# Kernel optimization log

Hardware: AMD Instinct MI355X
Metric: run time of the kernel (lower is better)

Reference implementation:

```python
import jax, jax.numpy as jnp
import numpy as np

GROUP_SIZE = 128


def setup_inputs() -> dict:
    key = jax.random.key(0)
    k0, k1, k2, k3 = jax.random.split(key, 4)
    B, S, I, O, G = 4, 2048, 4096, 11008, GROUP_SIZE
    x = jax.random.normal(k0, (B, S, I), dtype=jnp.float32)
    # int4 values in [-8, 7]
    qweight = jax.random.randint(k1, (O, I), -8, 8, dtype=jnp.int32)
    # group-wise positive scales, shape [O, I // G]
    scales = jax.random.uniform(k2, (O, I // G), dtype=jnp.float32,
                                minval=1e-3, maxval=2e-2)
    bias = jax.random.normal(k3, (O,), dtype=jnp.float32) * 0.01
    return {"x": x, "qweight": qweight, "scales": scales, "bias": bias}


def reference(x, qweight, scales, bias):
    # bits == 4, quantized path: group-wise dequant then linear
    O, I = qweight.shape
    G = GROUP_SIZE
    w = qweight.reshape(O, I // G, G).astype(x.dtype) * scales[:, :, None].astype(x.dtype)
    w = w.reshape(O, I)  # dequantized weight [O, I]
    # F.linear: y = x @ w.T + bias
    return jnp.einsum('bsi,oi->bso', x, w) + bias.astype(x.dtype)
```

## Files before the change

### kernel.cpp

```cpp
#include <hip/hip_runtime.h>
#include <hip/hip_bf16.h>


typedef __bf16 bf16_t;
typedef __bf16 bf16x8 __attribute__((ext_vector_type(8)));
typedef float f32x4 __attribute__((ext_vector_type(4)));
typedef int ix4 __attribute__((ext_vector_type(4)));
typedef __attribute__((address_space(3))) unsigned char lds_byte;
typedef __attribute__((address_space(1))) unsigned char gmem_byte;

__global__ void prep_kernel(const float* __restrict__ x, int* __restrict__ xq,
                            float* __restrict__ sx,
                            const int* __restrict__ qw, const float* __restrict__ sc,
                            float* __restrict__ tw, int* __restrict__ wq,
                            int M, int I, int NG) {
  __shared__ float red[256];
  const int b = blockIdx.x;
  const int t = threadIdx.x;
  if (b < M) {
    const float* row = x + (size_t)b * I;
    float mx = 0.f;
    for (int c = t * 4; c < I; c += 1024) {
      const float4 f = *reinterpret_cast<const float4*>(row + c);
      mx = fmaxf(mx, fmaxf(fmaxf(fabsf(f.x), fabsf(f.y)), fmaxf(fabsf(f.z), fabsf(f.w))));
    }
    red[t] = mx;
    __syncthreads();
#pragma unroll
    for (int s = 128; s > 0; s >>= 1) {
      if (t < s) red[t] = fmaxf(red[t], red[t + s]);
      __syncthreads();
    }
    const float rm = fmaxf(red[0], 1e-30f);
    if (t == 0) sx[b] = rm * (1.f / 127.f);
    const float inv = 127.f / rm;
    int* orow = xq + (size_t)b * (I >> 2);
    for (int c = t * 4; c < I; c += 1024) {
      const float4 f = *reinterpret_cast<const float4*>(row + c);
      const int b0 = (int)rintf(f.x * inv), b1 = (int)rintf(f.y * inv);
      const int b2 = (int)rintf(f.z * inv), b3 = (int)rintf(f.w * inv);
      orow[c >> 2] = (b0 & 255) | ((b1 & 255) << 8) | ((b2 & 255) << 16) | (b3 << 24);
    }
  } else {
    const int n = b - M;
    const float* srow = sc + (size_t)n * NG;
    float mx = 0.f;
    for (int g = t; g < NG; g += 256) mx = fmaxf(mx, srow[g]);
    red[t] = mx;
    __syncthreads();
#pragma unroll
    for (int s = 128; s > 0; s >>= 1) {
      if (t < s) red[t] = fmaxf(red[t], red[t + s]);
      __syncthreads();
    }
    const float tn = fmaxf(red[0], 1e-30f) * (8.f / 127.f);
    if (t == 0) tw[n] = tn;
    const float itn = 1.f / tn;
    const int* qrow = qw + (size_t)n * I;
    int* orow = wq + (size_t)n * (I >> 2);
    for (int k0 = t * 16; k0 < I; k0 += 4096) {
      const float f = srow[k0 >> 7] * itn;
      const int4* p = reinterpret_cast<const int4*>(qrow + k0);
      const int4 q0 = p[0], q1 = p[1], q2 = p[2], q3 = p[3];
      int v[16];
      v[0] = (int)rintf((float)q0.x * f); v[1] = (int)rintf((float)q0.y * f);
      v[2] = (int)rintf((float)q0.z * f); v[3] = (int)rintf((float)q0.w * f);
      v[4] = (int)rintf((float)q1.x * f); v[5] = (int)rintf((float)q1.y * f);
      v[6] = (int)rintf((float)q1.z * f); v[7] = (int)rintf((float)q1.w * f);
      v[8] = (int)rintf((float)q2.x * f); v[9] = (int)rintf((float)q2.y * f);
      v[10] = (int)rintf((float)q2.z * f); v[11] = (int)rintf((float)q2.w * f);
      v[12] = (int)rintf((float)q3.x * f); v[13] = (int)rintf((float)q3.y * f);
      v[14] = (int)rintf((float)q3.z * f); v[15] = (int)rintf((float)q3.w * f);
      int4 o;
      o.x = (v[0] & 255) | ((v[1] & 255) << 8) | ((v[2] & 255) << 16) | (v[3] << 24);
      o.y = (v[4] & 255) | ((v[5] & 255) << 8) | ((v[6] & 255) << 16) | (v[7] << 24);
      o.z = (v[8] & 255) | ((v[9] & 255) << 8) | ((v[10] & 255) << 16) | (v[11] << 24);
      o.w = (v[12] & 255) | ((v[13] & 255) << 8) | ((v[14] & 255) << 16) | (v[15] << 24);
      *reinterpret_cast<int4*>(orow + (k0 >> 2)) = o;
    }
  }
}


#define WAITV(n) asm volatile("s_waitcnt vmcnt(" #n ")" ::: "memory")
#define WAITL(n) asm volatile("s_waitcnt lgkmcnt(" #n ")" ::: "memory")
#define BAR() __builtin_amdgcn_s_barrier()
#define SETP(n) __builtin_amdgcn_s_setprio(n)

#define RD_T(DB) do { \
  _Pragma("unroll") \
  for (int m_ = 0; m_ < 2; ++m_) { \
    aF[m_][0] = *reinterpret_cast<const ix4*>(&ldsb[(DB) + aRd + (unsigned)(m_ * 16) * 128u + ks0]); \
    aF[m_][1] = *reinterpret_cast<const ix4*>(&ldsb[(DB) + aRd + (unsigned)(m_ * 16) * 128u + ks1]); \
  } \
  _Pragma("unroll") \
  for (int n_ = 0; n_ < 4; ++n_) { \
    bF[n_][0] = *reinterpret_cast<const ix4*>(&ldsb[(DB) + 16384u + bRd + (unsigned)(n_ * 16) * 128u + ks0]); \
    bF[n_][1] = *reinterpret_cast<const ix4*>(&ldsb[(DB) + 16384u + bRd + (unsigned)(n_ * 16) * 128u + ks1]); \
  } \
} while (0)

#define STG(BASE, P, tau) do { \
  __builtin_amdgcn_global_load_lds((const gmem_byte*)((P) + (size_t)(tau) * 128), \
                                   (lds_byte*)&ldsb[(BASE) + wOff], 16, 0, 0); \
  __builtin_amdgcn_global_load_lds((const gmem_byte*)((P) + (size_t)64 * K + (size_t)(tau) * 128), \
                                   (lds_byte*)&ldsb[(BASE) + 8192u + wOff], 16, 0, 0); \
} while (0)

#define MM_T() do { \
  _Pragma("unroll") \
  for (int m_ = 0; m_ < 2; ++m_) \
  _Pragma("unroll") \
  for (int n_ = 0; n_ < 4; ++n_) { \
    acc[m_][n_] = __builtin_amdgcn_mfma_i32_16x16x64_i8(aF[m_][0], bF[n_][0], acc[m_][n_], 0, 0, 0); \
    acc[m_][n_] = __builtin_amdgcn_mfma_i32_16x16x64_i8(aF[m_][1], bF[n_][1], acc[m_][n_], 0, 0, 0); \
  } \
} while (0)

__launch_bounds__(512, 4)
__global__ void gemm128_i8_kernel(const char* __restrict__ A, const char* __restrict__ B,
                                  const float* __restrict__ sx, const float* __restrict__ tw,
                                  const float* __restrict__ bias, float* __restrict__ C,
                                  int M, int N, int K) {
  __shared__ __align__(16) unsigned char ldsb[65536];

  const int tid = threadIdx.x;
  const int lane = tid & 63;
  const int w = tid >> 6;
  const int wr = w >> 1;
  const int wc = w & 1;

  const int MT = M >> 7;
  int mt, nt;
  const int bid = blockIdx.x;
  if ((MT & 7) == 0) {
    const int xcd = bid & 7, idx = bid >> 3;
    const int mpx = MT >> 3;
    nt = idx / mpx;
    mt = xcd * mpx + (idx - nt * mpx);
  } else {
    mt = bid % MT;
    nt = bid / MT;
  }
  const int m0 = mt << 7, n0 = nt << 7;

  const int srow8 = lane >> 3;
  const int scol16 = (lane & 7) ^ (srow8 & 7);
  const char* aP = A + (size_t)(m0 + w * 8 + srow8) * K + scol16 * 16;
  const char* bP = B + (size_t)(n0 + w * 8 + srow8) * K + scol16 * 16;
  const unsigned wOff = (unsigned)w * 1024u;

  const unsigned fr = lane & 15;
  const unsigned hi16 = (unsigned)lane >> 4;
  const unsigned sw_ = (fr & 7u) << 4;
  const unsigned ks0 = (hi16 * 16u) ^ sw_;
  const unsigned ks1 = (64u + hi16 * 16u) ^ sw_;
  const unsigned aRd = ((unsigned)(wr * 32) + fr) * 128u;
  const unsigned bRd = ((unsigned)(wc * 64) + fr) * 128u;

  ix4 acc[2][4];
#pragma unroll
  for (int i = 0; i < 2; ++i)
#pragma unroll
    for (int j = 0; j < 4; ++j) acc[i][j] = (ix4){0, 0, 0, 0};

  ix4 aF[2][2], bF[4][2];

  const int NITER = K >> 7;

  STG(0u, aP, 0); STG(16384u, bP, 0);
  STG(32768u, aP, 1); STG(49152u, bP, 1);
  WAITV(4);
  BAR();

  for (int it = 0; it < (NITER >> 1) - 1; ++it) {
    const int t = 2 * it;
    RD_T(0u);
    WAITL(0);
    BAR();
    STG(0u, aP, t + 2); STG(16384u, bP, t + 2);
    SETP(1); MM_T(); SETP(0);
    WAITV(4);
    BAR();
    RD_T(32768u);
    WAITL(0);
    BAR();
    STG(32768u, aP, t + 3); STG(49152u, bP, t + 3);
    SETP(1); MM_T(); SETP(0);
    WAITV(4);
    BAR();
  }
  {
    RD_T(0u);
    WAITV(0);
    BAR();
    WAITL(0);
    SETP(1); MM_T(); SETP(0);
    RD_T(32768u);
    WAITL(0);
    SETP(1); MM_T(); SETP(0);
  }

  const int row0 = m0 + wr * 32 + ((lane >> 4) << 2);
  const int col0 = n0 + wc * 64 + (lane & 15);
  float sxc[2][4];
#pragma unroll
  for (int m_ = 0; m_ < 2; ++m_) {
    const int rbase = row0 + m_ * 16;
#pragma unroll
    for (int r = 0; r < 4; ++r) sxc[m_][r] = sx[rbase + r];
  }
#pragma unroll
  for (int n_ = 0; n_ < 4; ++n_) {
    const int n = col0 + n_ * 16;
    const float tn = tw[n];
    const float bv = bias[n];
#pragma unroll
    for (int m_ = 0; m_ < 2; ++m_) {
      const int rbase = row0 + m_ * 16;
#pragma unroll
      for (int r = 0; r < 4; ++r)
        C[(size_t)(rbase + r) * N + n] = sxc[m_][r] * tn * (float)acc[m_][n_][r] + bv;
    }
  }
}

__global__ void cvt_x_kernel(const float* __restrict__ x, bf16_t* __restrict__ xb, long n8) {
  const long stride = (long)gridDim.x * blockDim.x;
  for (long i = (long)blockIdx.x * blockDim.x + threadIdx.x; i < n8; i += stride) {
    const float4* p = reinterpret_cast<const float4*>(x + i * 8);
    const float4 f0 = p[0];
    const float4 f1 = p[1];
    bf16x8 o;
    o[0] = (bf16_t)f0.x; o[1] = (bf16_t)f0.y; o[2] = (bf16_t)f0.z; o[3] = (bf16_t)f0.w;
    o[4] = (bf16_t)f1.x; o[5] = (bf16_t)f1.y; o[6] = (bf16_t)f1.z; o[7] = (bf16_t)f1.w;
    *reinterpret_cast<bf16x8*>(xb + i * 8) = o;
  }
}

__global__ void deq_w_kernel(const int* __restrict__ qw, const float* __restrict__ sc,
                             bf16_t* __restrict__ wb, int I, int G) {
  const int n = blockIdx.y;
  const int kb = blockIdx.x * blockDim.x + threadIdx.x;
  const int k = kb * 8;
  if (k >= I) return;
  const float s = sc[(size_t)n * (I / G) + k / G];
  const int4* qp = reinterpret_cast<const int4*>(qw + (size_t)n * I + k);
  const int4 q0 = qp[0];
  const int4 q1 = qp[1];
  bf16x8 o;
  o[0] = (bf16_t)((float)q0.x * s);
  o[1] = (bf16_t)((float)q0.y * s);
  o[2] = (bf16_t)((float)q0.z * s);
  o[3] = (bf16_t)((float)q0.w * s);
  o[4] = (bf16_t)((float)q1.x * s);
  o[5] = (bf16_t)((float)q1.y * s);
  o[6] = (bf16_t)((float)q1.z * s);
  o[7] = (bf16_t)((float)q1.w * s);
  *reinterpret_cast<bf16x8*>(wb + (size_t)n * I + k) = o;
}

#define BM 128
#define BK 32
__launch_bounds__(256)
__global__ void gemm_bt_kernel(const bf16_t* __restrict__ A, const bf16_t* __restrict__ B,
                               const float* __restrict__ bias, float* __restrict__ C,
                               int M, int N, int K) {
  __shared__ __align__(16) bf16_t As[2][BM * BK];
  __shared__ __align__(16) bf16_t Bs[2][BM * BK];
  const int tid = threadIdx.x;
  const int lane = tid & 63;
  const int w = tid >> 6;
  const int wr = w >> 1;
  const int wc = w & 1;
  const int m0 = blockIdx.y * BM;
  const int n0 = blockIdx.x * BM;
  const int srow = lane >> 2;
  const int schunk = lane & 3;
  f32x4 acc[4][4];
  const f32x4 zero = {0.f, 0.f, 0.f, 0.f};
#pragma unroll
  for (int i = 0; i < 4; ++i)
#pragma unroll
    for (int j = 0; j < 4; ++j) acc[i][j] = zero;
  const int nt = K / BK;
  auto stage = [&](int t, int buf) {
    const int k0 = t * BK;
#pragma unroll
    for (int j = 0; j < 2; ++j) {
      const int row = w * 32 + j * 16;
      const bf16_t* ga = A + (size_t)(m0 + row + srow) * K + k0 + schunk * 8;
      __builtin_amdgcn_global_load_lds((const gmem_byte*)ga, (lds_byte*)&As[buf][row * BK], 16, 0, 0);
      const bf16_t* gb = B + (size_t)(n0 + row + srow) * K + k0 + schunk * 8;
      __builtin_amdgcn_global_load_lds((const gmem_byte*)gb, (lds_byte*)&Bs[buf][row * BK], 16, 0, 0);
    }
  };
  auto compute = [&](int buf) {
    bf16x8 af[4], bfr[4];
    const int fr2 = lane & 15;
    const int kc = (lane >> 4) * 8;
#pragma unroll
    for (int i = 0; i < 4; ++i) {
      af[i] = *reinterpret_cast<const bf16x8*>(&As[buf][(wr * 64 + i * 16 + fr2) * BK + kc]);
      bfr[i] = *reinterpret_cast<const bf16x8*>(&Bs[buf][(wc * 64 + i * 16 + fr2) * BK + kc]);
    }
#pragma unroll
    for (int i = 0; i < 4; ++i)
#pragma unroll
      for (int j = 0; j < 4; ++j)
        acc[i][j] = __builtin_amdgcn_mfma_f32_16x16x32_bf16(af[i], bfr[j], acc[i][j], 0, 0, 0);
  };
  stage(0, 0);
  __syncthreads();
  int cur = 0;
  for (int t = 0; t < nt - 1; ++t) {
    stage(t + 1, cur ^ 1);
    compute(cur);
    __syncthreads();
    cur ^= 1;
  }
  compute(cur);
#pragma unroll
  for (int j = 0; j < 4; ++j) {
    const int n = n0 + wc * 64 + j * 16 + (lane & 15);
    const float bv = bias[n];
#pragma unroll
    for (int i = 0; i < 4; ++i) {
      const int mbase = m0 + wr * 64 + i * 16 + (lane >> 4) * 4;
#pragma unroll
      for (int r = 0; r < 4; ++r)
        C[(size_t)(mbase + r) * N + n] = acc[i][j][r] + bv;
    }
  }
}

extern "C" void kernel_launch(void* const* d_in, const int* in_sizes, int n_in,
                              void* d_out, int out_size, void* d_ws, size_t ws_size,
                              hipStream_t stream) {
  const float* x = (const float*)d_in[0];
  const int* qw = (const int*)d_in[1];
  const float* sc = (const float*)d_in[2];
  const float* bias = (const float*)d_in[3];
  float* out = (float*)d_out;

  const long O = in_sizes[3];
  const long I = in_sizes[1] / O;
  const long M = in_sizes[0] / I;
  const long G = I / (in_sizes[2] / O);
  const long NG = I / G;

  const size_t i8need = (size_t)(M + O) * I + 4 * (size_t)(M + O);
  const long NITER = I >> 7;
  const bool i8ok = ((M & 127) == 0) && ((O & 127) == 0) && ((I & 127) == 0) &&
                    (G == 128) && (NITER >= 4) && ((NITER & 1) == 0) &&
                    (ws_size >= i8need);
  if (i8ok) {
    char* xq = (char*)d_ws;
    char* wq = xq + (size_t)M * I;
    float* sx = (float*)(wq + (size_t)O * I);
    float* tw = sx + M;
    prep_kernel<<<(unsigned)(M + O), 256, 0, stream>>>(x, (int*)xq, sx, qw, sc, tw,
                                                       (int*)wq, (int)M, (int)I, (int)NG);
    const int nwg = (int)((M >> 7) * (O >> 7));
    gemm128_i8_kernel<<<nwg, 512, 0, stream>>>(xq, wq, sx, tw, bias, out, (int)M, (int)O, (int)I);
  } else {
    bf16_t* xb = (bf16_t*)d_ws;
    bf16_t* wb = xb + (size_t)M * I;
    if (ws_size < (size_t)(M + O) * I * sizeof(bf16_t)) return;
    cvt_x_kernel<<<2048, 256, 0, stream>>>(x, xb, M * I / 8);
    dim3 dgrid((unsigned)((I / 8 + 255) / 256), (unsigned)O);
    deq_w_kernel<<<dgrid, 256, 0, stream>>>(qw, sc, wb, (int)I, (int)G);
    dim3 ggrid((unsigned)(O / BM), (unsigned)(M / BM));
    gemm_bt_kernel<<<ggrid, 256, 0, stream>>>(xb, wb, bias, out, (int)M, (int)O, (int)I);
  }
}
```

Measured before the change: 483.1 us.

## Double-buffer B fragments in registers and interleave LDS reads with MFMAs

Splits the B fragment registers into two sets (even and odd tiles). The LDS reads for the next tile's B fragments are issued inside the MFMA cluster of the current tile, and sched_group_barrier hints pair two MFMAs with one LDS read. The A fragment read is moved to just after each cluster, and the barrier and wait structure is reworked around this software pipeline. The aim is to hide LDS read latency behind matrix math; in exchange it needs about 32 more VGPRs under a 4-waves-per-SIMD bound, which risks spills, and it waits for all outstanding global loads (vmcnt 0) before each barrier.

Result: slower. 515.2 us (+6.6%).

```diff
diff --git a/kernel.cpp b/kernel.cpp
--- a/kernel.cpp
+++ b/kernel.cpp
@@ -86,17 +86,36 @@
 #define WAITL(n) asm volatile("s_waitcnt lgkmcnt(" #n ")" ::: "memory")
 #define BAR() __builtin_amdgcn_s_barrier()
 #define SETP(n) __builtin_amdgcn_s_setprio(n)
-
-#define RD_T(DB) do { \
+#define SGB __builtin_amdgcn_sched_group_barrier
+
+#define RD_A(DB) do { \
   _Pragma("unroll") \
   for (int m_ = 0; m_ < 2; ++m_) { \
     aF[m_][0] = *reinterpret_cast<const ix4*>(&ldsb[(DB) + aRd + (unsigned)(m_ * 16) * 128u + ks0]); \
     aF[m_][1] = *reinterpret_cast<const ix4*>(&ldsb[(DB) + aRd + (unsigned)(m_ * 16) * 128u + ks1]); \
   } \
+} while (0)
+
+#define CLUSTER(BC, BN, DBN) do { \
   _Pragma("unroll") \
-  for (int n_ = 0; n_ < 4; ++n_) { \
-    bF[n_][0] = *reinterpret_cast<const ix4*>(&ldsb[(DB) + 16384u + bRd + (unsigned)(n_ * 16) * 128u + ks0]); \
-    bF[n_][1] = *reinterpret_cast<const ix4*>(&ldsb[(DB) + 16384u + bRd + (unsigned)(n_ * 16) * 128u + ks1]); \
+  for (int p_ = 0; p_ < 8; ++p_) { \
+    const int m_ = p_ >> 2, n_ = p_ & 3; \
+    acc[m_][n_] = __builtin_amdgcn_mfma_i32_16x16x64_i8(aF[m_][0], BC[n_][0], acc[m_][n_], 0, 0, 0); \
+    acc[m_][n_] = __builtin_amdgcn_mfma_i32_16x16x64_i8(aF[m_][1], BC[n_][1], acc[m_][n_], 0, 0, 0); \
+    const int rn_ = p_ >> 1, rs_ = p_ & 1; \
+    BN[rn_][rs_] = *reinterpret_cast<const ix4*>( \
+      &ldsb[(DBN) + 16384u + bRd + (unsigned)(rn_ * 16) * 128u + (rs_ ? ks1 : ks0)]); \
+  } \
+  _Pragma("unroll") \
+  for (int p_ = 0; p_ < 8; ++p_) { SGB(0x8, 2, 0); SGB(0x100, 1, 0); } \
+} while (0)
+
+#define CLUSTER_LAST(BC) do { \
+  _Pragma("unroll") \
+  for (int p_ = 0; p_ < 8; ++p_) { \
+    const int m_ = p_ >> 2, n_ = p_ & 3; \
+    acc[m_][n_] = __builtin_amdgcn_mfma_i32_16x16x64_i8(aF[m_][0], BC[n_][0], acc[m_][n_], 0, 0, 0); \
+    acc[m_][n_] = __builtin_amdgcn_mfma_i32_16x16x64_i8(aF[m_][1], BC[n_][1], acc[m_][n_], 0, 0, 0); \
   } \
 } while (0)
 
@@ -105,16 +124,6 @@
                                    (lds_byte*)&ldsb[(BASE) + wOff], 16, 0, 0); \
   __builtin_amdgcn_global_load_lds((const gmem_byte*)((P) + (size_t)64 * K + (size_t)(tau) * 128), \
                                    (lds_byte*)&ldsb[(BASE) + 8192u + wOff], 16, 0, 0); \
-} while (0)
-
-#define MM_T() do { \
-  _Pragma("unroll") \
-  for (int m_ = 0; m_ < 2; ++m_) \
-  _Pragma("unroll") \
-  for (int n_ = 0; n_ < 4; ++n_) { \
-    acc[m_][n_] = __builtin_amdgcn_mfma_i32_16x16x64_i8(aF[m_][0], bF[n_][0], acc[m_][n_], 0, 0, 0); \
-    acc[m_][n_] = __builtin_amdgcn_mfma_i32_16x16x64_i8(aF[m_][1], bF[n_][1], acc[m_][n_], 0, 0, 0); \
-  } \
 } while (0)
 
 __launch_bounds__(512, 4)
@@ -164,7 +173,7 @@
 #pragma unroll
     for (int j = 0; j < 4; ++j) acc[i][j] = (ix4){0, 0, 0, 0};
 
-  ix4 aF[2][2], bF[4][2];
+  ix4 aF[2][2], bE[4][2], bO[4][2];
 
   const int NITER = K >> 7;
 
@@ -172,33 +181,39 @@
   STG(32768u, aP, 1); STG(49152u, bP, 1);
   WAITV(4);
   BAR();
+  {
+#pragma unroll
+    for (int p_ = 0; p_ < 8; ++p_) {
+      const int rn_ = p_ >> 1, rs_ = p_ & 1;
+      bE[rn_][rs_] = *reinterpret_cast<const ix4*>(
+        &ldsb[16384u + bRd + (unsigned)(rn_ * 16) * 128u + (rs_ ? ks1 : ks0)]);
+    }
+  }
+  RD_A(0u);
+  WAITL(0);
 
   for (int it = 0; it < (NITER >> 1) - 1; ++it) {
     const int t = 2 * it;
-    RD_T(0u);
-    WAITL(0);
+    WAITV(0);
     BAR();
     STG(0u, aP, t + 2); STG(16384u, bP, t + 2);
-    SETP(1); MM_T(); SETP(0);
-    WAITV(4);
-    BAR();
-    RD_T(32768u);
+    SETP(1); CLUSTER(bE, bO, 32768u); SETP(0);
+    RD_A(32768u);
     WAITL(0);
+    WAITV(0);
     BAR();
     STG(32768u, aP, t + 3); STG(49152u, bP, t + 3);
-    SETP(1); MM_T(); SETP(0);
-    WAITV(4);
-    BAR();
+    SETP(1); CLUSTER(bO, bE, 0u); SETP(0);
+    RD_A(0u);
+    WAITL(0);
   }
   {
-    RD_T(0u);
     WAITV(0);
     BAR();
+    SETP(1); CLUSTER(bE, bO, 32768u); SETP(0);
+    RD_A(32768u);
     WAITL(0);
-    SETP(1); MM_T(); SETP(0);
-    RD_T(32768u);
-    WAITL(0);
-    SETP(1); MM_T(); SETP(0);
+    SETP(1); CLUSTER_LAST(bO); SETP(0);
   }
 
   const int row0 = m0 + wr * 32 + ((lane >> 4) << 2);
```
